# Performance work log

Hardware: AMD Instinct MI355X
Metric: run time of the kernel (lower is better)

## Reference

```python
import jax, jax.numpy as jnp
import numpy as np

R = 29          # GF_kernel_size_train
EPS = 1e-09     # loss_eps
SAMPLING = 8    # sampling_in_MSEloss
LAMBDA_TV = 0.1
LAMBDA_HESSIAN = 0.5
ISO = True      # isotropic_hessian
SIGMA = 1.0     # hessian_kernel_sigma (>0.5 -> generateHessianKernel, angle_offset=[0])


def _hessian_kernels():
    half = int(np.ceil(SIGMA * 6))
    t = np.linspace(-half, half, 2 * half + 1)
    X, Y = np.meshgrid(t, t, indexing='ij')
    g = np.exp(-(X ** 2 + Y ** 2) / (2 * SIGMA ** 2))
    dxx = (1.0 / (2 * np.pi * SIGMA ** 4)) * (X ** 2 / SIGMA ** 2 - 1) * g
    dxy = (1.0 / (2 * np.pi * SIGMA ** 6)) * (X * Y) * g
    dyy = dxx.T
    # Loss.__init__ unpacks generateHessianKernel's return (Gaussyy, Gaussxx, Gaussxy)
    # into (self.DGaussxx, self.DGaussyy, self.DGaussxy); angle_offset=[0] -> identity rotate.
    Gxx = dyy.astype(np.float32)[None, None]
    Gyy = dxx.astype(np.float32)[None, None]
    Gxy = dxy.astype(np.float32)[None, None]
    return jnp.asarray(Gxx), jnp.asarray(Gyy), jnp.asarray(Gxy)


def _conv(x, k):
    return jax.lax.conv_general_dilated(x, k, (1, 1), 'VALID',
                                        dimension_numbers=('NCHW', 'OIHW', 'NCHW'))


def _boxfilter(x, r):
    # F.pad(input, (r+1, r, r+1, r)) pads last two dims (left r+1, right r each)
    xp = jnp.pad(x, ((0, 0), (0, 0), (r + 1, r), (r + 1, r)))
    c = jnp.cumsum(xp, axis=3)
    d = c[:, :, :, 2 * r + 1:] - c[:, :, :, :-2 * r - 1]
    c2 = jnp.cumsum(d, axis=2)
    return c2[:, :, 2 * r + 1:, :] - c2[:, :, :-2 * r - 1, :]


def _guided_filter(x, y, r, eps):
    N = _boxfilter(jnp.ones_like(x), r)
    mean_x = _boxfilter(x, r) / N
    mean_y = _boxfilter(y, r) / N
    cov_xy = _boxfilter(x * y, r) / N - mean_x * mean_y
    var_x = _boxfilter(x * x, r) / N - mean_x * mean_x
    A = cov_xy / jnp.clip(var_x, EPS, None)
    b = mean_y - A * mean_x
    A = _boxfilter(A, r) / N
    b = _boxfilter(b, r) / N
    return A * x + b


def _tv(x, target, Dx, Dy):
    return jnp.abs(_conv(x, Dx)).sum() + jnp.abs(_conv(x - target, Dy)).sum()


def _hessian(x, target, Gxx, Gyy, Gxy):
    scale = 2.0 if ISO else 1.0
    return (jnp.abs(_conv(x, Gxx)).sum()
            + jnp.abs(_conv(x - target, Gyy)).sum()
            + (jnp.abs(_conv(x - target, Gxy)) * scale).sum())


def setup_inputs() -> dict:
    key = jax.random.key(0)
    ks = jax.random.split(key, 6)
    shape = (1, 1, 3072, 3072)
    Gxx, Gyy, Gxy = _hessian_kernels()
    return {
        'outputGNNraw': jax.random.normal(ks[0], shape, dtype=jnp.float32),
        'outputGNN': jax.random.normal(ks[1], shape, dtype=jnp.float32),
        'outputLR': jax.random.normal(ks[2], shape, dtype=jnp.float32),
        'smoothedTarget': jax.random.normal(ks[3], shape, dtype=jnp.float32),
        'targets': jax.random.normal(ks[4], shape, dtype=jnp.float32),
        'map': jax.random.uniform(ks[5], shape, dtype=jnp.float32),
        'Dx': jnp.array([[1.0, -1.0]], dtype=jnp.float32)[None, None],   # [1,1,1,2]
        'Dy': jnp.array([[1.0], [-1.0]], dtype=jnp.float32)[None, None], # [1,1,2,1]
        'DGaussxx': Gxx, 'DGaussyy': Gyy, 'DGaussxy': Gxy,
    }


def reference(outputGNNraw, outputGNN, outputLR, smoothedTarget, targets, map,
              Dx, Dy, DGaussxx, DGaussyy, DGaussxy):
    gf = _guided_filter(outputGNNraw, outputGNNraw, R, EPS)
    mse = (jnp.abs(smoothedTarget - gf).sum()
           + (jnp.abs(targets - outputGNN) * map)[:, :, ::SAMPLING, ::SAMPLING].sum())
    tv = _tv(outputGNN, targets, Dx, Dy) + _tv(outputLR, targets, Dx, Dy)
    hess = (_hessian(outputGNN, targets, DGaussxx, DGaussyy, DGaussxy)
            + _hessian(outputLR, targets, DGaussxx, DGaussyy, DGaussxy))
    return mse + LAMBDA_TV * tv + LAMBDA_HESSIAN * hess
```

## Files before the change

### kernel.cpp

```cpp
#include <hip/hip_runtime.h>
#include <math.h>

#define W    3072
#define HH   3072
#define HOUT 3060
#define TW   64
#define TH   56
#define RW   7
#define NW   8
#define XR   68
#define XTS  76
#define VTS  77
#define VTW  (RW*VTS)
#define GX   48
#define GY   55
#define GZ   2
#define NBLK (GX*GY*GZ)
#define NTHR (NBLK*512)
#define NSLOT 64
#define NSTG ((XR*19+511)/512)

struct HessTaps { float a[13]; float bb[13]; float m[13]; float n[13]; };

__device__ double g_slots[NSLOT * 32];

__global__ __launch_bounds__(512, 8) void hess_kernel(const float* __restrict__ Gnn,
                                                      const float* __restrict__ Lr,
                                                      const float* __restrict__ T,
                                                      const float* __restrict__ Xr,
                                                      const float* __restrict__ St,
                                                      const float* __restrict__ Mp,
                                                      HessTaps tp) {
  __shared__ float xt[XR * XTS];
  __shared__ float vt[NW * VTW];
  __shared__ float red[NW][3];
  const float* img = (blockIdx.z == 0) ? Gnn : Lr;
  int oy = blockIdx.y * TH, ox = blockIdx.x * TW;
  int t = threadIdx.x;
  int wv = t >> 6, ln = t & 63;
  int r0 = wv * RW;

  for (int idx = t; idx < XR * 19; idx += 512) {
    int r = idx / 19, g = idx - r * 19;
    int gr = oy + r, gc = ox + 4 * g;
    float4 v = {0.f, 0.f, 0.f, 0.f};
    if (gr < HH) {
      const float* p = &img[(size_t)gr * W + gc];
      if (gc + 3 < W) v = *(const float4*)p;
      else {
        if (gc < W)     v.x = p[0];
        if (gc + 1 < W) v.y = p[1];
        if (gc + 2 < W) v.z = p[2];
      }
    }
    *(float4*)&xt[r * XTS + 4 * g] = v;
  }

  float4 tr4[NSTG];
  #pragma unroll
  for (int k = 0; k < NSTG; ++k) {
    int idx = t + 512 * k;
    float4 v = {0.f, 0.f, 0.f, 0.f};
    if (idx < XR * 19) {
      int r = idx / 19, g = idx - r * 19;
      int gr = oy + r, gc = ox + 4 * g;
      if (gr < HH) {
        const float* p = &T[(size_t)gr * W + gc];
        if (gc + 3 < W) v = *(const float4*)p;
        else {
          if (gc < W)     v.x = p[0];
          if (gc + 1 < W) v.y = p[1];
          if (gc + 2 < W) v.z = p[2];
        }
      }
    }
    tr4[k] = v;
  }

  int bid = (blockIdx.z * GY + blockIdx.y) * GX + blockIdx.x;
  int i0 = bid * 512 + t;
  const int n4 = (W * HH) / 4;
  float4 ga0 = {0.f, 0.f, 0.f, 0.f}, gb0 = ga0;
  bool has0 = (i0 < n4);
  if (has0) { ga0 = ((const float4*)Xr)[i0]; gb0 = ((const float4*)St)[i0]; }
  float mT = 0.f, mG = 0.f, mM = 0.f;
  bool hasm = (i0 < 384 * 384);
  if (hasm) {
    int si = i0 / 384, sj = i0 - si * 384;
    int id = si * 8 * W + sj * 8;
    mT = T[id]; mG = Gnn[id]; mM = Mp[id];
  }
  __builtin_amdgcn_sched_barrier(0);

  __syncthreads();

  float tvl = 0.f;
  float hl  = 0.f;

  {
    int gc = ox + ln;
    if (gc < W - 1) {
      #pragma unroll
      for (int i = 0; i < RW; ++i) {
        int r = r0 + i;
        if (oy + r < HH)
          tvl += fabsf(xt[r * XTS + ln] - xt[r * XTS + ln + 1]);
      }
    }
  }

  #define VPASS(TAP)                                                        \
    {                                                                       \
        \
      float oA[RW];                                                         \
      _Pragma("unroll")                                                     \
      for (int i = 0; i < RW; ++i) oA[i] = 0.f;                             \
      _Pragma("unroll")                                                     \
      for (int u = 0; u < RW + 12; ++u) {                                   \
        float xA = xt[(r0 + u) * XTS + ln];                                 \
        _Pragma("unroll")                                                   \
        for (int i = 0; i < RW; ++i) {                                      \
          int kk = u - i;                                                   \
          if (kk >= 0 && kk <= 12) oA[i] = fmaf((TAP)[kk], xA, oA[i]);      \
        }                                                                   \
      }                                                                     \
      float* vw = &vt[wv * VTW + ln];                                       \
      _Pragma("unroll")                                                     \
      for (int i = 0; i < RW; ++i) vw[i * VTS] = oA[i];                     \
                     \
      _Pragma("unroll")                                                     \
      for (int k = 0; k < 2; ++k) {                                         \
        int o = ln + 64 * k;                                                \
        if (o < 12 * RW) {                                                  \
          int row = o / 12, hc = o - row * 12;                              \
          const float* xp = &xt[(r0 + row) * XTS + 64 + hc];                \
          float s = 0.f;                                                    \
          _Pragma("unroll")                                                 \
          for (int u = 0; u < 13; ++u) s = fmaf((TAP)[u], xp[u * XTS], s);  \
          vt[wv * VTW + row * VTS + 64 + hc] = s;                           \
        }                                                                   \
      }                                                                     \
    }

  #define HSECOND(TAP, WGT)                                                 \
    {                                                                       \
      int r8 = ln >> 3, cg = ln & 7;                                        \
      if (r8 < RW) {                                                        \
        const float* vrow = &vt[wv * VTW + r8 * VTS + cg * 8];              \
        float o_[8];                                                        \
        _Pragma("unroll")                                                   \
        for (int jj = 0; jj < 8; ++jj) o_[jj] = 0.f;                        \
        _Pragma("unroll")                                                   \
        for (int j = 0; j < 20; ++j) {                                      \
          float v = vrow[j];                                                \
          _Pragma("unroll")                                                 \
          for (int jj = 0; jj < 8; ++jj) {                                  \
            int kk = j - jj;                                                \
            if (kk >= 0 && kk <= 12) o_[jj] = fmaf((TAP)[kk], v, o_[jj]);   \
          }                                                                 \
        }                                                                   \
        int gr = oy + r0 + r8;                                              \
        int gc0 = ox + cg * 8;                                              \
        float wr = (gr < HOUT) ? (WGT) : 0.f;                               \
        _Pragma("unroll")                                                   \
        for (int jj = 0; jj < 8; ++jj) {                                    \
          float m_ = (gc0 + jj < HOUT) ? wr : 0.f;                          \
          hl = fmaf(m_, fabsf(o_[jj]), hl);                                 \
        }                                                                   \
      }                                                                     \
    }

  VPASS(tp.bb);
  HSECOND(tp.a, 1.0f);

  __syncthreads();
  #pragma unroll
  for (int k = 0; k < NSTG; ++k) {
    int idx = t + 512 * k;
    if (idx < XR * 19) {
      int r = idx / 19, g = idx - r * 19;
      float4 cur = *(float4*)&xt[r * XTS + 4 * g];
      cur.x -= tr4[k].x; cur.y -= tr4[k].y;
      cur.z -= tr4[k].z; cur.w -= tr4[k].w;
      *(float4*)&xt[r * XTS + 4 * g] = cur;
    }
  }
  __syncthreads();

  {
    int gc = ox + ln;
    if (gc < W) {
      #pragma unroll
      for (int i = 0; i < RW; ++i) {
        int r = r0 + i;
        if (oy + r < HH - 1)
          tvl += fabsf(xt[r * XTS + ln] - xt[(r + 1) * XTS + ln]);
      }
    }
  }

  VPASS(tp.a);
  HSECOND(tp.bb, 1.0f);

  VPASS(tp.m);
  HSECOND(tp.n, 2.0f);

  float gm = 0.f;
  if (has0)
    gm = fabsf(gb0.x - ga0.x) + fabsf(gb0.y - ga0.y)
       + fabsf(gb0.z - ga0.z) + fabsf(gb0.w - ga0.w);
  if (hasm) gm += fabsf(mT - mG) * mM;

  #pragma unroll
  for (int o = 32; o > 0; o >>= 1) {
    gm  += __shfl_down(gm,  o, 64);
    tvl += __shfl_down(tvl, o, 64);
    hl  += __shfl_down(hl,  o, 64);
  }
  if (ln == 0) { red[wv][0] = gm; red[wv][1] = tvl; red[wv][2] = hl; }
  __syncthreads();
  if (t == 0) {
    float s0 = 0.f, s1 = 0.f, s2 = 0.f;
    #pragma unroll
    for (int w = 0; w < NW; ++w) {
      s0 += red[w][0]; s1 += red[w][1]; s2 += red[w][2];
    }
    int slot = bid & (NSLOT - 1);
    double* base = g_slots + (size_t)slot * 32;
    unsafeAtomicAdd(base,      (double)s0);
    unsafeAtomicAdd(base + 8,  (double)s1);
    unsafeAtomicAdd(base + 16, (double)s2);
  }
}

__global__ __launch_bounds__(64) void finalize_kernel(float* __restrict__ out) {
  int t = threadIdx.x;
  double* b = g_slots + (size_t)t * 32;
  double s0 = b[0];  b[0]  = 0.0;
  double s1 = b[8];  b[8]  = 0.0;
  double s3 = b[16]; b[16] = 0.0;
  #pragma unroll
  for (int o = 32; o > 0; o >>= 1) {
    s0 += __shfl_down(s0, o, 64);
    s1 += __shfl_down(s1, o, 64);
    s3 += __shfl_down(s3, o, 64);
  }
  if (t == 0) out[0] = (float)(s0 + 0.1 * s1 + 0.5 * s3);
}

extern "C" void kernel_launch(void* const* d_in, const int* in_sizes, int n_in,
                              void* d_out, int out_size, void* d_ws, size_t ws_size,
                              hipStream_t stream) {
  const float* xraw = (const float*)d_in[0];
  const float* gnn  = (const float*)d_in[1];
  const float* lr   = (const float*)d_in[2];
  const float* st   = (const float*)d_in[3];
  const float* tg   = (const float*)d_in[4];
  const float* mp   = (const float*)d_in[5];
  float* out = (float*)d_out;

  HessTaps tp;
  const double PI2 = 6.283185307179586476925287;
  for (int k = 0; k < 13; ++k) {
    double tt = (double)(k - 6);
    double g = exp(-0.5 * tt * tt);
    tp.a[k]  = (float)((tt * tt - 1.0) * g / PI2);
    tp.bb[k] = (float)g;
    tp.m[k]  = (float)(tt * g / PI2);
    tp.n[k]  = (float)(tt * g);
  }

  hess_kernel<<<dim3(GX, GY, GZ), 512, 0, stream>>>(gnn, lr, tg, xraw, st, mp,
                                                    tp);
  finalize_kernel<<<1, 64, 0, stream>>>(out);
}
```

Before: 251.2 us.

## Fuse two vertical Hessian passes and specialize interior blocks without bounds masks

Merges the vertical convolution passes for the a and m taps into one pass over the shared tile, so each tile value is read from LDS once for both filters. The m results are held in registers and written to the scratch buffer after the bb horizontal pass. The kernel body is also templated on an edge flag, so interior blocks skip all boundary comparisons. This raises register pressure (extra accumulators) and duplicates code, which could hurt occupancy under the 512x8 launch bounds.

```diff
diff --git a/kernel.cpp b/kernel.cpp
--- a/kernel.cpp
+++ b/kernel.cpp
@@ -1,5 +1,6 @@
 #include <hip/hip_runtime.h>
 #include <math.h>
+#include <type_traits>
 
 #define W    3072
 #define HH   3072
@@ -16,7 +17,6 @@
 #define GY   55
 #define GZ   2
 #define NBLK (GX*GY*GZ)
-#define NTHR (NBLK*512)
 #define NSLOT 64
 #define NSTG ((XR*19+511)/512)
 
@@ -97,21 +97,8 @@
   float tvl = 0.f;
   float hl  = 0.f;
 
-  {
-    int gc = ox + ln;
-    if (gc < W - 1) {
-      #pragma unroll
-      for (int i = 0; i < RW; ++i) {
-        int r = r0 + i;
-        if (oy + r < HH)
-          tvl += fabsf(xt[r * XTS + ln] - xt[r * XTS + ln + 1]);
-      }
-    }
-  }
-
   #define VPASS(TAP)                                                        \
     {                                                                       \
-        \
       float oA[RW];                                                         \
       _Pragma("unroll")                                                     \
       for (int i = 0; i < RW; ++i) oA[i] = 0.f;                             \
@@ -127,7 +114,6 @@
       float* vw = &vt[wv * VTW + ln];                                       \
       _Pragma("unroll")                                                     \
       for (int i = 0; i < RW; ++i) vw[i * VTS] = oA[i];                     \
-                     \
       _Pragma("unroll")                                                     \
       for (int k = 0; k < 2; ++k) {                                         \
         int o = ln + 64 * k;                                                \
@@ -142,6 +128,46 @@
       }                                                                     \
     }
 
+  #define VPASS2(TAPA, TAPM)                                                \
+    {                                                                       \
+      float oA[RW];                                                         \
+      _Pragma("unroll")                                                     \
+      for (int i = 0; i < RW; ++i) { oA[i] = 0.f; oM[i] = 0.f; }            \
+      _Pragma("unroll")                                                     \
+      for (int u = 0; u < RW + 12; ++u) {                                   \
+        float xA = xt[(r0 + u) * XTS + ln];                                 \
+        _Pragma("unroll")                                                   \
+        for (int i = 0; i < RW; ++i) {                                      \
+          int kk = u - i;                                                   \
+          if (kk >= 0 && kk <= 12) {                                        \
+            oA[i] = fmaf((TAPA)[kk], xA, oA[i]);                            \
+            oM[i] = fmaf((TAPM)[kk], xA, oM[i]);                            \
+          }                                                                 \
+        }                                                                   \
+      }                                                                     \
+      float* vw = &vt[wv * VTW + ln];                                       \
+      _Pragma("unroll")                                                     \
+      for (int i = 0; i < RW; ++i) vw[i * VTS] = oA[i];                     \
+      _Pragma("unroll")                                                     \
+      for (int k = 0; k < 2; ++k) {                                         \
+        smv[k] = 0.f;                                                       \
+        int o = ln + 64 * k;                                                \
+        if (o < 12 * RW) {                                                  \
+          int row = o / 12, hc = o - row * 12;                              \
+          const float* xp = &xt[(r0 + row) * XTS + 64 + hc];                \
+          float sA = 0.f, sM = 0.f;                                         \
+          _Pragma("unroll")                                                 \
+          for (int u = 0; u < 13; ++u) {                                    \
+            float xv = xp[u * XTS];                                         \
+            sA = fmaf((TAPA)[u], xv, sA);                                   \
+            sM = fmaf((TAPM)[u], xv, sM);                                   \
+          }                                                                 \
+          vt[wv * VTW + row * VTS + 64 + hc] = sA;                          \
+          smv[k] = sM;                                                      \
+        }                                                                   \
+      }                                                                     \
+    }
+
   #define HSECOND(TAP, WGT)                                                 \
     {                                                                       \
       int r8 = ln >> 3, cg = ln & 7;                                        \
@@ -159,51 +185,84 @@
             if (kk >= 0 && kk <= 12) o_[jj] = fmaf((TAP)[kk], v, o_[jj]);   \
           }                                                                 \
         }                                                                   \
-        int gr = oy + r0 + r8;                                              \
+        float wr = (WGT);                                                   \
+        if (MSK) { int gr = oy + r0 + r8; if (gr >= HOUT) wr = 0.f; }       \
         int gc0 = ox + cg * 8;                                              \
-        float wr = (gr < HOUT) ? (WGT) : 0.f;                               \
         _Pragma("unroll")                                                   \
         for (int jj = 0; jj < 8; ++jj) {                                    \
-          float m_ = (gc0 + jj < HOUT) ? wr : 0.f;                          \
+          float m_ = wr;                                                    \
+          if (MSK) { if (gc0 + jj >= HOUT) m_ = 0.f; }                      \
           hl = fmaf(m_, fabsf(o_[jj]), hl);                                 \
         }                                                                   \
       }                                                                     \
     }
 
-  VPASS(tp.bb);
-  HSECOND(tp.a, 1.0f);
-
-  __syncthreads();
-  #pragma unroll
-  for (int k = 0; k < NSTG; ++k) {
-    int idx = t + 512 * k;
-    if (idx < XR * 19) {
-      int r = idx / 19, g = idx - r * 19;
-      float4 cur = *(float4*)&xt[r * XTS + 4 * g];
-      cur.x -= tr4[k].x; cur.y -= tr4[k].y;
-      cur.z -= tr4[k].z; cur.w -= tr4[k].w;
-      *(float4*)&xt[r * XTS + 4 * g] = cur;
-    }
-  }
-  __syncthreads();
-
-  {
-    int gc = ox + ln;
-    if (gc < W) {
+  auto body = [&](auto mskc) {
+    constexpr int MSK = decltype(mskc)::value;
+    float oM[RW], smv[2];
+
+    {
+      int gc = ox + ln;
+      if (!MSK || gc < W - 1) {
+        #pragma unroll
+        for (int i = 0; i < RW; ++i) {
+          int r = r0 + i;
+          if (!MSK || oy + r < HH)
+            tvl += fabsf(xt[r * XTS + ln] - xt[r * XTS + ln + 1]);
+        }
+      }
+    }
+
+    VPASS(tp.bb);
+    HSECOND(tp.a, 1.0f);
+
+    __syncthreads();
+    #pragma unroll
+    for (int k = 0; k < NSTG; ++k) {
+      int idx = t + 512 * k;
+      if (idx < XR * 19) {
+        int r = idx / 19, g = idx - r * 19;
+        float4 cur = *(float4*)&xt[r * XTS + 4 * g];
+        cur.x -= tr4[k].x; cur.y -= tr4[k].y;
+        cur.z -= tr4[k].z; cur.w -= tr4[k].w;
+        *(float4*)&xt[r * XTS + 4 * g] = cur;
+      }
+    }
+    __syncthreads();
+
+    {
+      int gc = ox + ln;
+      if (!MSK || gc < W) {
+        #pragma unroll
+        for (int i = 0; i < RW; ++i) {
+          int r = r0 + i;
+          if (!MSK || oy + r < HH - 1)
+            tvl += fabsf(xt[r * XTS + ln] - xt[(r + 1) * XTS + ln]);
+        }
+      }
+    }
+
+    VPASS2(tp.a, tp.m);
+    HSECOND(tp.bb, 1.0f);
+    {
+      float* vw = &vt[wv * VTW + ln];
       #pragma unroll
-      for (int i = 0; i < RW; ++i) {
-        int r = r0 + i;
-        if (oy + r < HH - 1)
-          tvl += fabsf(xt[r * XTS + ln] - xt[(r + 1) * XTS + ln]);
-      }
-    }
-  }
-
-  VPASS(tp.a);
-  HSECOND(tp.bb, 1.0f);
-
-  VPASS(tp.m);
-  HSECOND(tp.n, 2.0f);
+      for (int i = 0; i < RW; ++i) vw[i * VTS] = oM[i];
+      #pragma unroll
+      for (int k = 0; k < 2; ++k) {
+        int o = ln + 64 * k;
+        if (o < 12 * RW) {
+          int row = o / 12, hc = o - row * 12;
+          vt[wv * VTW + row * VTS + 64 + hc] = smv[k];
+        }
+      }
+    }
+    HSECOND(tp.n, 2.0f);
+  };
+
+  bool edge = (blockIdx.x == GX - 1) || (blockIdx.y == GY - 1);
+  if (edge) body(std::integral_constant<int, 1>{});
+  else      body(std::integral_constant<int, 0>{});
 
   float gm = 0.f;
   if (has0)
```

Measured after the change: 330.0 us. 31.4% more time.
